# Kernel tuning notes

Hardware: AMD Instinct MI355X
Metric: run time of the kernel (lower is better)

The kernel has to match this reference:

```python
import jax, jax.numpy as jnp
import numpy as np

EMBD = 768
N_HEADS = 12
HEAD_SIZE = EMBD // N_HEADS  # 64


def setup_inputs() -> dict:
    key = jax.random.key(0)
    kx, kq, kk, kv = jax.random.split(key, 4)
    B, S = 4, 4096
    x = jax.random.normal(kx, (B, S, EMBD), dtype=jnp.float32)
    # nn.Linear(embd, head_size, bias=False): y = x @ W.T with W [head_size, embd].
    # We store the transposed weight [embd, head_size] and apply x @ Wq, same math.
    scale = 1.0 / np.sqrt(EMBD)
    Wq = jax.random.normal(kq, (EMBD, HEAD_SIZE), dtype=jnp.float32) * scale
    Wk = jax.random.normal(kk, (EMBD, HEAD_SIZE), dtype=jnp.float32) * scale
    Wv = jax.random.normal(kv, (EMBD, HEAD_SIZE), dtype=jnp.float32) * scale
    return {"x": x, "Wq": Wq, "Wk": Wk, "Wv": Wv}


def reference(x, Wq, Wk, Wv):
    # q, k, v: [B, S, head_size]
    q = jnp.einsum("bse,eh->bsh", x, Wq)
    k = jnp.einsum("bse,eh->bsh", x, Wk)
    v = jnp.einsum("bse,eh->bsh", x, Wv)
    scale = jnp.asarray(HEAD_SIZE, q.dtype) ** -0.5
    # scores: [B, S, S]
    scores = jnp.einsum("bqh,bkh->bqk", q, k) * scale
    S = x.shape[1]
    causal = jnp.tril(jnp.ones((S, S), dtype=bool))
    scores = jnp.where(causal, scores, jnp.asarray(-jnp.inf, scores.dtype))
    weights = jax.nn.softmax(scores, axis=-1)
    # attn_dropout = 0.0 -> identity
    out = jnp.einsum("bqk,bkh->bqh", weights, v)  # [B, S, head_size]
    return out
```

## Files before the change

kernel.cpp:

```cpp
#include <hip/hip_runtime.h>

#define EMBD 768
#define HS 64
#define S_LEN 4096
#define BK 64

typedef __attribute__((ext_vector_type(8))) short short8;
typedef __attribute__((ext_vector_type(4))) short short4_t;
typedef __attribute__((ext_vector_type(4))) float f32x4;
typedef unsigned short ushort_t;
typedef unsigned int uint_t;

static __device__ __forceinline__ ushort_t f2bf(float f) {
    union { float f; unsigned u; } x; x.f = f;
    unsigned r = x.u + 0x7fffu + ((x.u >> 16) & 1u);
    return (ushort_t)(r >> 16);
}

static __device__ __forceinline__ float bf2f(ushort_t u) {
    union { float f; uint_t u; } x; x.u = ((uint_t)u) << 16; return x.f;
}

static __device__ __forceinline__ uint_t cvt_pk_bf16(float lo, float hi) {
    uint_t r;
    asm volatile("v_cvt_pk_bf16_f32 %0, %1, %2" : "=v"(r) : "v"(lo), "v"(hi));
    return r;
}

static __device__ __forceinline__ short8 pack_bf8(float4 a, float4 b) {
    union { short8 s; uint_t u[4]; } r;
    r.u[0] = cvt_pk_bf16(a.x, a.y); r.u[1] = cvt_pk_bf16(a.z, a.w);
    r.u[2] = cvt_pk_bf16(b.x, b.y); r.u[3] = cvt_pk_bf16(b.z, b.w);
    return r.s;
}

static __device__ __forceinline__ void gl_lds16(const void* g, void* l) {
    __builtin_amdgcn_global_load_lds(
        (const __attribute__((address_space(1))) unsigned int*)g,
        (__attribute__((address_space(3))) unsigned int*)l, 16, 0, 0);
}

__global__ __launch_bounds__(256) void wprep_kernel(
    const float* __restrict__ Wq, const float* __restrict__ Wk, const float* __restrict__ Wv,
    ushort_t* __restrict__ Wt)
{
    __shared__ float ws[64][65];
    const int blk  = blockIdx.x;
    const int widx = blk / 12, kblk = blk % 12;
    const float* W = (widx == 0) ? Wq : (widx == 1) ? Wk : Wv;
    const int k0 = kblk * 64;
    const int t  = threadIdx.x;
    const int r  = t >> 2, c0 = (t & 3) * 16;
#pragma unroll
    for (int i = 0; i < 4; ++i) {
        float4 v = *(const float4*)(W + (size_t)(k0 + r) * HS + c0 + i * 4);
        ws[c0 + i*4 + 0][r] = v.x; ws[c0 + i*4 + 1][r] = v.y;
        ws[c0 + i*4 + 2][r] = v.z; ws[c0 + i*4 + 3][r] = v.w;
    }
    __syncthreads();
    const int c = t >> 2, kc = (t & 3) * 16;
    ushort_t* dst = Wt + (size_t)(widx * 64 + c) * EMBD + k0 + kc;
#pragma unroll
    for (int i = 0; i < 4; ++i) {
        short4_t p = {(short)f2bf(ws[c][kc + i*4 + 0]), (short)f2bf(ws[c][kc + i*4 + 1]),
                      (short)f2bf(ws[c][kc + i*4 + 2]), (short)f2bf(ws[c][kc + i*4 + 3])};
        *(short4_t*)(dst + i * 4) = p;
    }
}

__global__ __launch_bounds__(512) void qkv_kernel(
    const float* __restrict__ x, const ushort_t* __restrict__ Wt,
    ushort_t* __restrict__ Qg, ushort_t* __restrict__ Kg, ushort_t* __restrict__ Vtg)
{
    __shared__ char xA[2][4096];
    __shared__ char Wl[2][12288];
    __shared__ float Vs[32][65];
    const int t    = threadIdx.x;
    const int w    = t >> 6;
    const int lane = t & 63;
    const int l15  = lane & 15;
    const int l4   = lane >> 4;
    const int mg   = w >> 2;
    const int cg   = w & 3;
    const int row0 = blockIdx.x * 32;

    const float* g1srcA = 0; const ushort_t* g1srcW = 0;
    if (t < 256) {
        const int row = t >> 3, gi = t & 7;
        g1srcA = x + (size_t)(row0 + row) * EMBD + ((gi ^ (row & 7)) << 2);
    } else {
        const int c = (t - 256) >> 2, gi = t & 3;
        const int sc = (c & 3) ^ ((c >> 2) & 3);
        g1srcW = Wt + (size_t)c * EMBD + ((gi ^ sc) << 3);
    }
    const int c2 = 64 + (t >> 2), gi2 = t & 3;
    const int sc2 = (c2 & 3) ^ ((c2 >> 2) & 3);
    const ushort_t* g2srcW = Wt + (size_t)c2 * EMBD + ((gi2 ^ sc2) << 3);

    auto stage = [&](int kt, int buf) {
        const int xo = kt * 32;
        if (t < 256) gl_lds16(g1srcA + xo, xA[buf] + (w & 3) * 1024);
        else         gl_lds16(g1srcW + xo, Wl[buf] + (w - 4) * 1024);
        gl_lds16(g2srcW + xo, Wl[buf] + 4096 + w * 1024);
    };

    const int ar = mg * 16 + l15;
    const int wc0 = cg * 48 + l15;
    const int wc1 = wc0 + 16, wc2 = wc0 + 32;
    const int swc0 = l4 ^ (wc0 & 3) ^ ((wc0 >> 2) & 3);
    const int swc1 = l4 ^ (wc1 & 3) ^ ((wc1 >> 2) & 3);
    const int swc2 = l4 ^ (wc2 & 3) ^ ((wc2 >> 2) & 3);

    f32x4 acc[3];
#pragma unroll
    for (int j = 0; j < 3; ++j) acc[j] = (f32x4){0.f, 0.f, 0.f, 0.f};

    stage(0, 0);
    __syncthreads();

#pragma unroll
    for (int kt = 0; kt < 24; ++kt) {
        const int cur = kt & 1;
        if (kt < 23) stage(kt + 1, cur ^ 1);
        const char* Ab = xA[cur];
        const char* Wb = Wl[cur];
        float4 a0 = *(const float4*)(Ab + ar * 128 + (((2 * l4)     ^ (ar & 7)) << 4));
        float4 a1 = *(const float4*)(Ab + ar * 128 + (((2 * l4 + 1) ^ (ar & 7)) << 4));
        short8 af = pack_bf8(a0, a1);
        short8 wf0 = *(const short8*)(Wb + wc0 * 64 + (swc0 << 4));
        short8 wf1 = *(const short8*)(Wb + wc1 * 64 + (swc1 << 4));
        short8 wf2 = *(const short8*)(Wb + wc2 * 64 + (swc2 << 4));
        acc[0] = __builtin_amdgcn_mfma_f32_16x16x32_bf16(af, wf0, acc[0], 0, 0, 0);
        acc[1] = __builtin_amdgcn_mfma_f32_16x16x32_bf16(af, wf1, acc[1], 0, 0, 0);
        acc[2] = __builtin_amdgcn_mfma_f32_16x16x32_bf16(af, wf2, acc[2], 0, 0, 0);
        if (kt < 23) __syncthreads();
    }

    const int lrow = mg * 16 + l4 * 4;
    const size_t grow = (size_t)row0 + lrow;
#pragma unroll
    for (int ct = 0; ct < 3; ++ct) {
        const int cbase = cg * 48 + ct * 16;
        const int sel   = cbase >> 6;
        const int cloc  = (cbase & 63) + l15;
#pragma unroll
        for (int r = 0; r < 4; ++r) {
            const float v = acc[ct][r];
            if (sel == 0)      Qg[(grow + r) * HS + cloc] = f2bf(v * 0.125f);
            else if (sel == 1) Kg[(grow + r) * HS + cloc] = f2bf(v);
            else               Vs[lrow + r][cloc] = v;
        }
    }
    __syncthreads();
    {
        const int vcol = t >> 3, vr0 = (t & 7) * 4;
        const int bb = row0 >> 12, s0 = row0 & 4095;
        union { short4_t s; uint_t u[2]; } vp;
        vp.u[0] = cvt_pk_bf16(Vs[vr0][vcol],     Vs[vr0 + 1][vcol]);
        vp.u[1] = cvt_pk_bf16(Vs[vr0 + 2][vcol], Vs[vr0 + 3][vcol]);
        *(short4_t*)(Vtg + ((size_t)bb * HS + vcol) * S_LEN + s0 + vr0) = vp.s;
    }
}

__global__ __launch_bounds__(256) void attn_kernel(
    const ushort_t* __restrict__ Qg, const ushort_t* __restrict__ Kg,
    const ushort_t* __restrict__ Vtg,
    ushort_t* __restrict__ pacc, float* __restrict__ pm, float* __restrict__ pl)
{
    __shared__ char smem[40960];
    const int t    = threadIdx.x;
    const int w    = t >> 6;
    const int lane = t & 63;
    const int l15  = lane & 15;
    const int l4   = lane >> 4;

    const int g     = blockIdx.x;
    const int b     = g >> 7;
    const int inner = g & 127;
    const int jp    = inner >> 2;
    const int v     = inner & 3;

    const ushort_t* Kb_ = Kg  + (size_t)b * S_LEN * HS;
    const ushort_t* Vb_ = Vtg + (size_t)b * HS * S_LEN;
    const ushort_t* Qb_ = Qg  + (size_t)b * S_LEN * HS;

    char* myP = smem + 32768 + w * 2048;
    const int psw = (l15 & 7) << 4;

    auto stage = [&](int k0, int db) {
#pragma unroll
        for (int i = 0; i < 2; ++i) {
            const int row = w * 16 + i * 8 + (lane >> 3);
            const int c   = lane & 7;
            gl_lds16(Kb_ + (size_t)(k0 + row) * HS + ((c ^ (row & 7)) * 8),
                     smem + db * 8192 + w * 2048 + i * 1024);
            gl_lds16(Vb_ + (size_t)row * S_LEN + k0 + ((c ^ (row & 7)) * 8),
                     smem + 16384 + db * 8192 + w * 2048 + i * 1024);
        }
    };

    auto run_phase = [&](int r, int pidx) {
        const int q0r = r * BK;
        const int nt  = r + 1;
        const int q   = q0r + w * 16 + l15;
        const ushort_t* qrow = Qb_ + (size_t)q * HS;
        short8 qf0 = *(const short8*)(qrow + l4 * 8);
        short8 qf1 = *(const short8*)(qrow + 32 + l4 * 8);
        f32x4 acc[4];
#pragma unroll
        for (int j = 0; j < 4; ++j) acc[j] = (f32x4){0.f,0.f,0.f,0.f};
        float mm = -3e38f, ls = 0.f;

        __syncthreads();
        if (v < nt) stage(v * BK, 0);
        int db = 0;
        for (int tt = v; tt < nt; tt += 4, db ^= 1) {
            __syncthreads();
            if (tt + 4 < nt) stage((tt + 4) * BK, db ^ 1);
            const char* Kt  = smem + db * 8192;
            const char* Vt2 = smem + 16384 + db * 8192;

            f32x4 sT[4];
#pragma unroll
            for (int st = 0; st < 4; ++st) {
                const int krow = st * 16 + l15;
                const char* krb = Kt + krow * 128;
                const int sw = krow & 7;
                short8 kc0 = *(const short8*)(krb + ((l4 ^ sw) << 4));
                short8 kc1 = *(const short8*)(krb + (((4 + l4) ^ sw) << 4));
                f32x4 z = (f32x4){0.f,0.f,0.f,0.f};
                z = __builtin_amdgcn_mfma_f32_16x16x32_bf16(kc0, qf0, z, 0, 0, 0);
                z = __builtin_amdgcn_mfma_f32_16x16x32_bf16(kc1, qf1, z, 0, 0, 0);
                sT[st] = z;
            }
            if (tt == r) {
#pragma unroll
                for (int st = 0; st < 4; ++st)
#pragma unroll
                    for (int rr = 0; rr < 4; ++rr)
                        if (tt * BK + st * 16 + l4 * 4 + rr > q) sT[st][rr] = -3e38f;
            }
            float a0 = fmaxf(fmaxf(sT[0][0], sT[0][1]), fmaxf(sT[0][2], sT[0][3]));
            float a1 = fmaxf(fmaxf(sT[1][0], sT[1][1]), fmaxf(sT[1][2], sT[1][3]));
            float a2 = fmaxf(fmaxf(sT[2][0], sT[2][1]), fmaxf(sT[2][2], sT[2][3]));
            float a3 = fmaxf(fmaxf(sT[3][0], sT[3][1]), fmaxf(sT[3][2], sT[3][3]));
            float mt = fmaxf(fmaxf(a0, a1), fmaxf(a2, a3));
            if (__any(mt > mm + 8.f)) {
                mt = fmaxf(mt, __shfl_xor(mt, 16));
                mt = fmaxf(mt, __shfl_xor(mt, 32));
                float mn = fmaxf(mm, mt);
                float corr = __expf(mm - mn);
                ls *= corr;
#pragma unroll
                for (int ds = 0; ds < 4; ++ds)
#pragma unroll
                    for (int rr = 0; rr < 4; ++rr) acc[ds][rr] *= corr;
                mm = mn;
            }
            char* pr = myP + l15 * 128;
            float la = 0.f;
#pragma unroll
            for (int st = 0; st < 4; ++st) {
                float p0 = __expf(sT[st][0] - mm);
                float p1 = __expf(sT[st][1] - mm);
                float p2 = __expf(sT[st][2] - mm);
                float p3 = __expf(sT[st][3] - mm);
                la += (p0 + p1) + (p2 + p3);
                uint2 pk; pk.x = cvt_pk_bf16(p0, p1); pk.y = cvt_pk_bf16(p2, p3);
                *(uint2*)(pr + ((st * 32 + l4 * 8) ^ psw)) = pk;
            }
            ls += la;
            short8 pb0 = *(const short8*)(pr + ((l4 * 16) ^ psw));
            short8 pb1 = *(const short8*)(pr + ((64 + l4 * 16) ^ psw));
#pragma unroll
            for (int ds = 0; ds < 4; ++ds) {
                const int vrow = ds * 16 + l15;
                const char* vrb = Vt2 + vrow * 128;
                const int sw2 = vrow & 7;
                short8 v0 = *(const short8*)(vrb + ((l4 ^ sw2) << 4));
                short8 v1 = *(const short8*)(vrb + (((4 + l4) ^ sw2) << 4));
                acc[ds] = __builtin_amdgcn_mfma_f32_16x16x32_bf16(v0, pb0, acc[ds], 0, 0, 0);
                acc[ds] = __builtin_amdgcn_mfma_f32_16x16x32_bf16(v1, pb1, acc[ds], 0, 0, 0);
            }
        }

        ls += __shfl_xor(ls, 16);
        ls += __shfl_xor(ls, 32);
        ushort_t* pa = pacc + ((size_t)pidx * 64 + w * 16 + l15) * 64 + l4 * 4;
#pragma unroll
        for (int ds = 0; ds < 4; ++ds) {
            uint2 pk;
            pk.x = cvt_pk_bf16(acc[ds][0], acc[ds][1]);
            pk.y = cvt_pk_bf16(acc[ds][2], acc[ds][3]);
            *(uint2*)(pa + ds * 16) = pk;
        }
        if (l4 == 0) {
            pm[pidx * 64 + w * 16 + l15] = mm;
            pl[pidx * 64 + w * 16 + l15] = ls;
        }
    };

    run_phase(jp,      (b * 64 + jp) * 4 + v);
    run_phase(63 - jp, (b * 64 + 63 - jp) * 4 + v);
}

__global__ __launch_bounds__(256) void combine_kernel(
    const ushort_t* __restrict__ pacc, const float* __restrict__ pm, const float* __restrict__ pl,
    float* __restrict__ out)
{
    const int g   = blockIdx.x;
    const int t   = threadIdx.x;
    const int row = t >> 2;
    const int d0  = (t & 3) * 16;
    float mv[4], lv[4];
#pragma unroll
    for (int p = 0; p < 4; ++p) {
        mv[p] = pm[(g * 4 + p) * 64 + row];
        lv[p] = pl[(g * 4 + p) * 64 + row];
    }
    float ms = fmaxf(fmaxf(mv[0], mv[1]), fmaxf(mv[2], mv[3]));
    float e[4], ll = 0.f;
#pragma unroll
    for (int p = 0; p < 4; ++p) { e[p] = __expf(mv[p] - ms); ll += lv[p] * e[p]; }
    const float inv = 1.f / ll;
    float o[16];
#pragma unroll
    for (int i = 0; i < 16; ++i) o[i] = 0.f;
#pragma unroll
    for (int p = 0; p < 4; ++p) {
        const ushort_t* src = pacc + ((size_t)(g * 4 + p) * 64 + row) * 64 + d0;
        short8 s0 = *(const short8*)(src);
        short8 s1 = *(const short8*)(src + 8);
#pragma unroll
        for (int i = 0; i < 8; ++i) {
            o[i]     += bf2f((ushort_t)s0[i]) * e[p];
            o[8 + i] += bf2f((ushort_t)s1[i]) * e[p];
        }
    }
    float4* op = (float4*)&out[((size_t)g * 64 + row) * 64 + d0];
#pragma unroll
    for (int i = 0; i < 4; ++i)
        op[i] = make_float4(o[i*4] * inv, o[i*4+1] * inv, o[i*4+2] * inv, o[i*4+3] * inv);
}

extern "C" void kernel_launch(void* const* d_in, const int* in_sizes, int n_in,
                              void* d_out, int out_size, void* d_ws, size_t ws_size,
                              hipStream_t stream) {
    const float* x  = (const float*)d_in[0];
    const float* Wq = (const float*)d_in[1];
    const float* Wk = (const float*)d_in[2];
    const float* Wv = (const float*)d_in[3];
    float* out = (float*)d_out;

    const int rows = in_sizes[0] / EMBD;
    const int B    = rows / S_LEN;

    ushort_t* Qb = (ushort_t*)d_ws;
    ushort_t* Kb = Qb + (size_t)rows * HS;
    ushort_t* Vt = Kb + (size_t)rows * HS;
    ushort_t* Wt = Vt + (size_t)rows * HS;
    ushort_t* pacc = Wt + 192 * EMBD;
    float* pm = (float*)(pacc + (size_t)B * 64 * 4 * 64 * 64);
    float* pl = pm + (size_t)B * 64 * 4 * 64;

    hipLaunchKernelGGL(wprep_kernel, dim3(36), dim3(256), 0, stream, Wq, Wk, Wv, Wt);
    hipLaunchKernelGGL(qkv_kernel, dim3(rows / 32), dim3(512), 0, stream,
                       x, Wt, Qb, Kb, Vt);
    hipLaunchKernelGGL(attn_kernel, dim3(B * 128), dim3(256), 0, stream,
                       Qb, Kb, Vt, pacc, pm, pl);
    hipLaunchKernelGGL(combine_kernel, dim3(B * 64), dim3(256), 0, stream,
                       pacc, pm, pl, out);
}
```

Measured before the change: 54.88 us.

## Split attention KV range six ways and widen QKV projection k-tiles

The attention kernel now splits each query tile's key range across six blocks instead of four, with batch-interleaved block ordering. The grid grows from 512 to 768 blocks, which spreads the causal work more evenly across the GPU's CUs. The combine kernel is generalized to merge six partials, and workspace sizing is updated. The QKV projection now stages 64-wide k chunks, doing two MFMA steps per stage with new swizzles, which halves the number of barriers. The cost is more partial-result traffic and larger LDS use in the QKV kernel.

After: 50.80 us, median of 3. 1.08x faster.

```diff
diff --git a/kernel.cpp b/kernel.cpp
--- a/kernel.cpp
+++ b/kernel.cpp
@@ -4,6 +4,7 @@
 #define HS 64
 #define S_LEN 4096
 #define BK 64
+#define NPAR 6
 
 typedef __attribute__((ext_vector_type(8))) short short8;
 typedef __attribute__((ext_vector_type(4))) short short4_t;
@@ -72,8 +73,8 @@
     const float* __restrict__ x, const ushort_t* __restrict__ Wt,
     ushort_t* __restrict__ Qg, ushort_t* __restrict__ Kg, ushort_t* __restrict__ Vtg)
 {
-    __shared__ char xA[2][4096];
-    __shared__ char Wl[2][12288];
+    __shared__ char xA[2][8192];
+    __shared__ char Wl[2][24576];
     __shared__ float Vs[32][65];
     const int t    = threadIdx.x;
     const int w    = t >> 6;
@@ -84,32 +85,24 @@
     const int cg   = w & 3;
     const int row0 = blockIdx.x * 32;
 
-    const float* g1srcA = 0; const ushort_t* g1srcW = 0;
-    if (t < 256) {
-        const int row = t >> 3, gi = t & 7;
-        g1srcA = x + (size_t)(row0 + row) * EMBD + ((gi ^ (row & 7)) << 2);
-    } else {
-        const int c = (t - 256) >> 2, gi = t & 3;
-        const int sc = (c & 3) ^ ((c >> 2) & 3);
-        g1srcW = Wt + (size_t)c * EMBD + ((gi ^ sc) << 3);
-    }
-    const int c2 = 64 + (t >> 2), gi2 = t & 3;
-    const int sc2 = (c2 & 3) ^ ((c2 >> 2) & 3);
-    const ushort_t* g2srcW = Wt + (size_t)c2 * EMBD + ((gi2 ^ sc2) << 3);
+    const int arow_s = t >> 4, ag = t & 15;
+    const float* asrc = x + (size_t)(row0 + arow_s) * EMBD + ((ag ^ (arow_s & 15)) << 2);
+    const int wcs = t >> 3, wgs = t & 7;
+    const ushort_t* wsrc0 = Wt + (size_t)(wcs      ) * EMBD + ((wgs ^ (wcs & 7)) << 3);
+    const ushort_t* wsrc1 = Wt + (size_t)(wcs +  64) * EMBD + ((wgs ^ (wcs & 7)) << 3);
+    const ushort_t* wsrc2 = Wt + (size_t)(wcs + 128) * EMBD + ((wgs ^ (wcs & 7)) << 3);
 
     auto stage = [&](int kt, int buf) {
-        const int xo = kt * 32;
-        if (t < 256) gl_lds16(g1srcA + xo, xA[buf] + (w & 3) * 1024);
-        else         gl_lds16(g1srcW + xo, Wl[buf] + (w - 4) * 1024);
-        gl_lds16(g2srcW + xo, Wl[buf] + 4096 + w * 1024);
+        const int xo = kt * 64;
+        gl_lds16(asrc + xo,  xA[buf] + w * 1024);
+        gl_lds16(wsrc0 + xo, Wl[buf] + w * 1024);
+        gl_lds16(wsrc1 + xo, Wl[buf] + 8192 + w * 1024);
+        gl_lds16(wsrc2 + xo, Wl[buf] + 16384 + w * 1024);
     };
 
     const int ar = mg * 16 + l15;
     const int wc0 = cg * 48 + l15;
     const int wc1 = wc0 + 16, wc2 = wc0 + 32;
-    const int swc0 = l4 ^ (wc0 & 3) ^ ((wc0 >> 2) & 3);
-    const int swc1 = l4 ^ (wc1 & 3) ^ ((wc1 >> 2) & 3);
-    const int swc2 = l4 ^ (wc2 & 3) ^ ((wc2 >> 2) & 3);
 
     f32x4 acc[3];
 #pragma unroll
@@ -119,21 +112,26 @@
     __syncthreads();
 
 #pragma unroll
-    for (int kt = 0; kt < 24; ++kt) {
+    for (int kt = 0; kt < 12; ++kt) {
         const int cur = kt & 1;
-        if (kt < 23) stage(kt + 1, cur ^ 1);
+        if (kt < 11) stage(kt + 1, cur ^ 1);
         const char* Ab = xA[cur];
         const char* Wb = Wl[cur];
-        float4 a0 = *(const float4*)(Ab + ar * 128 + (((2 * l4)     ^ (ar & 7)) << 4));
-        float4 a1 = *(const float4*)(Ab + ar * 128 + (((2 * l4 + 1) ^ (ar & 7)) << 4));
-        short8 af = pack_bf8(a0, a1);
-        short8 wf0 = *(const short8*)(Wb + wc0 * 64 + (swc0 << 4));
-        short8 wf1 = *(const short8*)(Wb + wc1 * 64 + (swc1 << 4));
-        short8 wf2 = *(const short8*)(Wb + wc2 * 64 + (swc2 << 4));
-        acc[0] = __builtin_amdgcn_mfma_f32_16x16x32_bf16(af, wf0, acc[0], 0, 0, 0);
-        acc[1] = __builtin_amdgcn_mfma_f32_16x16x32_bf16(af, wf1, acc[1], 0, 0, 0);
-        acc[2] = __builtin_amdgcn_mfma_f32_16x16x32_bf16(af, wf2, acc[2], 0, 0, 0);
-        if (kt < 23) __syncthreads();
+#pragma unroll
+        for (int ks = 0; ks < 2; ++ks) {
+            const int gf = ks * 8 + 2 * l4;
+            float4 a0 = *(const float4*)(Ab + ar * 256 + (((gf    ) ^ l15) << 4));
+            float4 a1 = *(const float4*)(Ab + ar * 256 + (((gf + 1) ^ l15) << 4));
+            short8 af = pack_bf8(a0, a1);
+            const int gw = ks * 4 + l4;
+            short8 wf0 = *(const short8*)(Wb + wc0 * 128 + ((gw ^ (wc0 & 7)) << 4));
+            short8 wf1 = *(const short8*)(Wb + wc1 * 128 + ((gw ^ (wc1 & 7)) << 4));
+            short8 wf2 = *(const short8*)(Wb + wc2 * 128 + ((gw ^ (wc2 & 7)) << 4));
+            acc[0] = __builtin_amdgcn_mfma_f32_16x16x32_bf16(af, wf0, acc[0], 0, 0, 0);
+            acc[1] = __builtin_amdgcn_mfma_f32_16x16x32_bf16(af, wf1, acc[1], 0, 0, 0);
+            acc[2] = __builtin_amdgcn_mfma_f32_16x16x32_bf16(af, wf2, acc[2], 0, 0, 0);
+        }
+        if (kt < 11) __syncthreads();
     }
 
     const int lrow = mg * 16 + l4 * 4;
@@ -174,11 +172,11 @@
     const int l15  = lane & 15;
     const int l4   = lane >> 4;
 
-    const int g     = blockIdx.x;
-    const int b     = g >> 7;
-    const int inner = g & 127;
-    const int jp    = inner >> 2;
-    const int v     = inner & 3;
+    const int g  = blockIdx.x;
+    const int b  = g & 3;
+    const int rr = g >> 2;
+    const int jp = rr & 31;
+    const int v  = rr >> 5;
 
     const ushort_t* Kb_ = Kg  + (size_t)b * S_LEN * HS;
     const ushort_t* Vb_ = Vtg + (size_t)b * HS * S_LEN;
@@ -214,9 +212,9 @@
         __syncthreads();
         if (v < nt) stage(v * BK, 0);
         int db = 0;
-        for (int tt = v; tt < nt; tt += 4, db ^= 1) {
+        for (int tt = v; tt < nt; tt += NPAR, db ^= 1) {
             __syncthreads();
-            if (tt + 4 < nt) stage((tt + 4) * BK, db ^ 1);
+            if (tt + NPAR < nt) stage((tt + NPAR) * BK, db ^ 1);
             const char* Kt  = smem + db * 8192;
             const char* Vt2 = smem + 16384 + db * 8192;
 
@@ -237,8 +235,8 @@
 #pragma unroll
                 for (int st = 0; st < 4; ++st)
 #pragma unroll
-                    for (int rr = 0; rr < 4; ++rr)
-                        if (tt * BK + st * 16 + l4 * 4 + rr > q) sT[st][rr] = -3e38f;
+                    for (int rr2 = 0; rr2 < 4; ++rr2)
+                        if (tt * BK + st * 16 + l4 * 4 + rr2 > q) sT[st][rr2] = -3e38f;
             }
             float a0 = fmaxf(fmaxf(sT[0][0], sT[0][1]), fmaxf(sT[0][2], sT[0][3]));
             float a1 = fmaxf(fmaxf(sT[1][0], sT[1][1]), fmaxf(sT[1][2], sT[1][3]));
@@ -254,7 +252,7 @@
 #pragma unroll
                 for (int ds = 0; ds < 4; ++ds)
 #pragma unroll
-                    for (int rr = 0; rr < 4; ++rr) acc[ds][rr] *= corr;
+                    for (int rr2 = 0; rr2 < 4; ++rr2) acc[ds][rr2] *= corr;
                 mm = mn;
             }
             char* pr = myP + l15 * 128;
@@ -300,8 +298,8 @@
         }
     };
 
-    run_phase(jp,      (b * 64 + jp) * 4 + v);
-    run_phase(63 - jp, (b * 64 + 63 - jp) * 4 + v);
+    run_phase(jp,      (b * 64 + jp) * NPAR + v);
+    run_phase(63 - jp, (b * 64 + 63 - jp) * NPAR + v);
 }
 
 __global__ __launch_bounds__(256) void combine_kernel(
@@ -312,23 +310,25 @@
     const int t   = threadIdx.x;
     const int row = t >> 2;
     const int d0  = (t & 3) * 16;
-    float mv[4], lv[4];
-#pragma unroll
-    for (int p = 0; p < 4; ++p) {
-        mv[p] = pm[(g * 4 + p) * 64 + row];
-        lv[p] = pl[(g * 4 + p) * 64 + row];
-    }
-    float ms = fmaxf(fmaxf(mv[0], mv[1]), fmaxf(mv[2], mv[3]));
-    float e[4], ll = 0.f;
-#pragma unroll
-    for (int p = 0; p < 4; ++p) { e[p] = __expf(mv[p] - ms); ll += lv[p] * e[p]; }
+    float mv[NPAR], lv[NPAR];
+#pragma unroll
+    for (int p = 0; p < NPAR; ++p) {
+        mv[p] = pm[(g * NPAR + p) * 64 + row];
+        lv[p] = pl[(g * NPAR + p) * 64 + row];
+    }
+    float ms = mv[0];
+#pragma unroll
+    for (int p = 1; p < NPAR; ++p) ms = fmaxf(ms, mv[p]);
+    float e[NPAR], ll = 0.f;
+#pragma unroll
+    for (int p = 0; p < NPAR; ++p) { e[p] = __expf(mv[p] - ms); ll += lv[p] * e[p]; }
     const float inv = 1.f / ll;
     float o[16];
 #pragma unroll
     for (int i = 0; i < 16; ++i) o[i] = 0.f;
 #pragma unroll
-    for (int p = 0; p < 4; ++p) {
-        const ushort_t* src = pacc + ((size_t)(g * 4 + p) * 64 + row) * 64 + d0;
+    for (int p = 0; p < NPAR; ++p) {
+        const ushort_t* src = pacc + ((size_t)(g * NPAR + p) * 64 + row) * 64 + d0;
         short8 s0 = *(const short8*)(src);
         short8 s1 = *(const short8*)(src + 8);
 #pragma unroll
@@ -360,13 +360,13 @@
     ushort_t* Vt = Kb + (size_t)rows * HS;
     ushort_t* Wt = Vt + (size_t)rows * HS;
     ushort_t* pacc = Wt + 192 * EMBD;
-    float* pm = (float*)(pacc + (size_t)B * 64 * 4 * 64 * 64);
-    float* pl = pm + (size_t)B * 64 * 4 * 64;
+    float* pm = (float*)(pacc + (size_t)B * 64 * NPAR * 64 * 64);
+    float* pl = pm + (size_t)B * 64 * NPAR * 64;
 
     hipLaunchKernelGGL(wprep_kernel, dim3(36), dim3(256), 0, stream, Wq, Wk, Wv, Wt);
     hipLaunchKernelGGL(qkv_kernel, dim3(rows / 32), dim3(512), 0, stream,
                        x, Wt, Qb, Kb, Vt);
-    hipLaunchKernelGGL(attn_kernel, dim3(B * 128), dim3(256), 0, stream,
+    hipLaunchKernelGGL(attn_kernel, dim3(B * 32 * NPAR), dim3(256), 0, stream,
                        Qb, Kb, Vt, pacc, pm, pl);
     hipLaunchKernelGGL(combine_kernel, dim3(B * 64), dim3(256), 0, stream,
                        pacc, pm, pl, out);
```
